# Kernel tuning notes

Measured on AMD Instinct MI355X. Metric: run time of the kernel, lower is better.

The kernel has to match this reference:

```python
import jax, jax.numpy as jnp
import numpy as np

N = 100000
E = 6400000
GAMMA = 1.0
SUPPORT = 0.05


def cohesion_kernel(q, h):
    # piecewise Akinci cohesion kernel (Cd normalization is unused in the original)
    qm1_3_q3 = (q - 1.0) ** 3 * q ** 3
    k1 = 128.0 * qm1_3_q3 + 1.0   # q <= 0.5
    k2 = 64.0 * qm1_3_q3           # q > 0.5
    return -jnp.where(q <= 0.5, k1, k2)


def kernel_gradient(q, dist, h):
    # 2D Wendland C2 kernel gradient: W = 7/(pi h^2) (1-q)^4 (1+4q)
    C = 7.0 / (np.pi * h ** 2)
    dWdq = C * (-20.0 * q * jnp.clip(1.0 - q, 0.0, None) ** 3) / h
    return dWdq[:, None] * dist  # [E,2]


def setup_inputs() -> dict:
    key = jax.random.key(0)
    k1, k2, k3, k4, k5, k6, k7 = jax.random.split(key, 7)
    neighbors = jnp.stack([
        jax.random.randint(k1, (E,), 0, N),
        jax.random.randint(k2, (E,), 0, N),
    ], axis=0)  # [2,E] int
    fluidAreas = jax.random.uniform(k3, (N,), dtype=jnp.float32)
    fluidDensities = jax.random.uniform(k4, (N,), dtype=jnp.float32) + 0.5  # avoid div-by-0
    fluidRestDensity = jax.random.uniform(k5, (N,), dtype=jnp.float32) + 0.5
    fluidRadialDistances = jax.random.uniform(k6, (E,), dtype=jnp.float32)  # q in [0,1]
    fluidDistances = jax.random.normal(k7, (E, 2), dtype=jnp.float32)
    # normalize to unit direction vectors as in the SPH pipeline
    fluidDistances = fluidDistances / (jnp.linalg.norm(fluidDistances, axis=1, keepdims=True) + 1e-7)
    return {
        'neighbors': neighbors,
        'fluidAreas': fluidAreas,
        'fluidDensities': fluidDensities,
        'fluidRestDensity': fluidRestDensity,
        'fluidRadialDistances': fluidRadialDistances,
        'fluidDistances': fluidDistances,
    }


def reference(neighbors, fluidAreas, fluidDensities, fluidRestDensity,
              fluidRadialDistances, fluidDistances):
    i = neighbors[0]
    j = neighbors[1]

    # computeNormalFunction
    fac_n = fluidAreas[j] / fluidDensities[j]                  # [E]
    grad = kernel_gradient(fluidRadialDistances, fluidDistances, SUPPORT)  # [E,2]
    normals = SUPPORT * jax.ops.segment_sum(fac_n[:, None] * grad, i, num_segments=N)  # [N,2]

    # computeCurvatureForce
    curvature = -GAMMA * jax.ops.segment_sum(normals[i] - normals[j], i, num_segments=N)

    # computeCohesionForce
    fac_c = fluidAreas[j] * fluidRestDensity[j]                # [E]
    kern = cohesion_kernel(fluidRadialDistances, SUPPORT)      # [E]
    cohesion = -GAMMA * jax.ops.segment_sum((fac_c * kern)[:, None] * fluidDistances, i, num_segments=N)

    # both forces are accumulated into fluidAcceleration
    return curvature + cohesion
```

## Files before the change

### kernel.cpp

```cpp
#include <hip/hip_runtime.h>

constexpr int N_PART = 100000;
constexpr int N_EDGE = 6400000;
constexpr float SUPPORT = 0.05f;
constexpr float PI_F = 3.14159265358979323846f;

constexpr int CH_LOG2 = 12;
constexpr int CH      = 1 << CH_LOG2;
constexpr int NCH     = (N_EDGE + CH - 1) / CH;
constexpr int BIN_LOG2 = 12;
constexpr int BINSZ   = 1 << BIN_LOG2;
constexpr int NBIN    = (N_PART + BINSZ - 1) / BINSZ;
constexpr int BT_STRIDE = 32;
constexpr int G_ACC   = 40;
constexpr int ST_NW   = 8;
constexpr int MAXC    = 48;

__global__ __launch_bounds__(512) void prep_fac(
    const float* __restrict__ areas,
    const float* __restrict__ dens,
    const float* __restrict__ rest,
    float2* __restrict__ fac)
{
    int p = blockIdx.x * blockDim.x + threadIdx.x;
    if (p < N_PART)
        fac[p] = make_float2(areas[p] / dens[p], areas[p] * rest[p]);
}

__global__ __launch_bounds__(256) void zero2(float* __restrict__ a,
                                             float* __restrict__ b, int n) {
    int idx = blockIdx.x * blockDim.x + threadIdx.x;
    if (idx < n) { a[idx] = 0.0f; b[idx] = 0.0f; }
}

__global__ __launch_bounds__(512) void l1_sort(
    const int* __restrict__ nb,
    const float2* __restrict__ fac,
    const float* __restrict__ q,
    const float2* __restrict__ dist,
    unsigned* __restrict__ gpack,
    float2* __restrict__ gpay1,
    float2* __restrict__ gpay2,
    unsigned* __restrict__ btab)
{
    __shared__ unsigned rec_pack[CH];
    __shared__ float    rec_q[CH];
    __shared__ float    rec_dx[CH];
    __shared__ float    rec_dy[CH];
    __shared__ unsigned hist[ST_NW * NBIN];
    __shared__ unsigned curw[ST_NW * NBIN];
    __shared__ unsigned base[NBIN + 1];
    __shared__ unsigned bcnt[NBIN];

    const int t   = blockIdx.x;
    const int c0  = t * CH;
    const int len = min(CH, N_EDGE - c0);
    const int tid = threadIdx.x;
    const int wid = tid >> 6;

    for (int k = tid; k < ST_NW * NBIN; k += 512) hist[k] = 0u;

    unsigned iv[8], jv[8];
    float    qv[8], dxv[8], dyv[8];
    #pragma unroll
    for (int k = 0; k < 8; ++k) {
        int idx = tid + k * 512;
        if (idx < len) {
            iv[k] = (unsigned)nb[c0 + idx];
            jv[k] = (unsigned)nb[N_EDGE + c0 + idx];
            qv[k] = q[c0 + idx];
            float2 d = dist[c0 + idx];
            dxv[k] = d.x;
            dyv[k] = d.y;
        }
    }
    __syncthreads();

    #pragma unroll
    for (int k = 0; k < 8; ++k) {
        int idx = tid + k * 512;
        if (idx < len)
            atomicAdd(&hist[wid * NBIN + (iv[k] >> BIN_LOG2)], 1u);
    }
    __syncthreads();

    if (tid < NBIN) {
        unsigned run = 0;
        for (int w = 0; w < ST_NW; ++w) {
            curw[w * NBIN + tid] = run;
            run += hist[w * NBIN + tid];
        }
        bcnt[tid] = run;
    }
    __syncthreads();
    if (tid == 0) {
        unsigned run = 0;
        for (int b = 0; b < NBIN; ++b) { base[b] = run; run += bcnt[b]; }
        base[NBIN] = run;
    }
    __syncthreads();
    if (tid < ST_NW * NBIN) curw[tid] += base[tid % NBIN];
    if (tid < NBIN)  btab[t * BT_STRIDE + tid]  = base[tid];
    if (tid == NBIN) btab[t * BT_STRIDE + NBIN] = (unsigned)len;
    __syncthreads();

    #pragma unroll
    for (int k = 0; k < 8; ++k) {
        int idx = tid + k * 512;
        if (idx < len) {
            unsigned i   = iv[k];
            unsigned bin = i >> BIN_LOG2;
            unsigned r = atomicAdd(&curw[wid * NBIN + bin], 1u) & (CH - 1);
            rec_pack[r] = ((i & (BINSZ - 1)) << 17) | jv[k];
            rec_q[r]    = qv[k];
            rec_dx[r]   = dxv[k];
            rec_dy[r]   = dyv[k];
        }
    }
    __syncthreads();

    const float Cw = 7.0f / (PI_F * SUPPORT * SUPPORT);
    for (int p = tid; p < len; p += 512) {
        unsigned pack = rec_pack[p];
        float qq = rec_q[p];
        float dx = rec_dx[p], dy = rec_dy[p];
        unsigned j = pack & 0x1FFFFu;
        float2 f = fac[j];

        float omq  = fmaxf(1.0f - qq, 0.0f);
        float dWdq = Cw * (-20.0f * qq * omq * omq * omq) * (1.0f / SUPPORT);
        float s    = SUPPORT * f.x * dWdq;

        float qm1  = qq - 1.0f;
        float tt   = qm1 * qm1 * qm1 * qq * qq * qq;
        float kern = (qq <= 0.5f) ? fmaf(128.0f, tt, 1.0f) : 64.0f * tt;
        float fc   = f.y * kern;

        int o = c0 + p;
        gpack[o] = pack;
        gpay1[o] = make_float2(s * dx, s * dy);
        gpay2[o] = make_float2(fc * dx, fc * dy);
    }
}

__global__ __launch_bounds__(512) void passB(
    const unsigned* __restrict__ btab,
    const unsigned* __restrict__ gpack,
    const float2* __restrict__ gpay1,
    float* __restrict__ gnorm)
{
    __shared__ float accx[BINSZ];
    __shared__ float accy[BINSZ];
    __shared__ unsigned s_sb[MAXC], s_se[MAXC], s_ln[MAXC];
    const int b = blockIdx.x % NBIN;
    const int g = blockIdx.x / NBIN;
    const int wave = threadIdx.x >> 6;
    const int lane = threadIdx.x & 63;

    const int t0 = (int)((long long)g * NCH / G_ACC);
    const int t1 = (int)((long long)(g + 1) * NCH / G_ACC);
    const int nt = t1 - t0;

    for (int k = threadIdx.x; k < BINSZ; k += 512) { accx[k] = 0.0f; accy[k] = 0.0f; }
    for (int c = threadIdx.x; c < nt; c += 512) {
        s_sb[c] = btab[(t0 + c) * BT_STRIDE + b];
        s_se[c] = btab[(t0 + c) * BT_STRIDE + b + 1];
        s_ln[c] = btab[(t0 + c) * BT_STRIDE + NBIN];
    }
    __syncthreads();

    for (int c = wave; c < nt; c += 8) {
        const int c0  = (t0 + c) * CH;
        const unsigned ln = min(s_ln[c], (unsigned)CH);
        unsigned sb = min(s_sb[c], ln);
        unsigned se = min(s_se[c], ln);
        for (unsigned k = sb + lane; k < se; k += 64) {
            int o = c0 + (int)k;
            unsigned pk = gpack[o];
            float2 p = gpay1[o];
            unsigned loc = (pk >> 17) & (BINSZ - 1);
            atomicAdd(&accx[loc], p.x);
            atomicAdd(&accy[loc], p.y);
        }
    }
    __syncthreads();

    const int gbase = b * BINSZ;
    for (int k = threadIdx.x; k < BINSZ; k += 512) {
        int p = gbase + k;
        if (p < N_PART) {
            atomicAdd(&gnorm[2 * p],     accx[k]);
            atomicAdd(&gnorm[2 * p + 1], accy[k]);
        }
    }
}

__global__ __launch_bounds__(512) void passD(
    const unsigned* __restrict__ btab,
    const unsigned* __restrict__ gpack,
    const float2* __restrict__ gpay2,
    const float2* __restrict__ normals,
    float* __restrict__ gout)
{
    __shared__ float accx[BINSZ];
    __shared__ float accy[BINSZ];
    __shared__ unsigned s_sb[MAXC], s_se[MAXC], s_ln[MAXC];
    const int b = blockIdx.x % NBIN;
    const int g = blockIdx.x / NBIN;
    const int wave = threadIdx.x >> 6;
    const int lane = threadIdx.x & 63;

    const int t0 = (int)((long long)g * NCH / G_ACC);
    const int t1 = (int)((long long)(g + 1) * NCH / G_ACC);
    const int nt = t1 - t0;

    for (int k = threadIdx.x; k < BINSZ; k += 512) { accx[k] = 0.0f; accy[k] = 0.0f; }
    for (int c = threadIdx.x; c < nt; c += 512) {
        s_sb[c] = btab[(t0 + c) * BT_STRIDE + b];
        s_se[c] = btab[(t0 + c) * BT_STRIDE + b + 1];
        s_ln[c] = btab[(t0 + c) * BT_STRIDE + NBIN];
    }
    __syncthreads();

    const int gbase = b * BINSZ;
    for (int c = wave; c < nt; c += 8) {
        const int c0  = (t0 + c) * CH;
        const unsigned ln = min(s_ln[c], (unsigned)CH);
        unsigned sb = min(s_sb[c], ln);
        unsigned se = min(s_se[c], ln);
        for (unsigned k = sb + lane; k < se; k += 64) {
            int o = c0 + (int)k;
            unsigned pk = gpack[o];
            float2 coh = gpay2[o];
            unsigned loc = (pk >> 17) & (BINSZ - 1);
            unsigned j   = min(pk & 0x1FFFFu, (unsigned)(N_PART - 1));
            unsigned ii  = min((unsigned)(gbase + loc), (unsigned)(N_PART - 1));
            float2 nj = normals[j];
            float2 ni = normals[ii];
            atomicAdd(&accx[loc], nj.x - ni.x + coh.x);
            atomicAdd(&accy[loc], nj.y - ni.y + coh.y);
        }
    }
    __syncthreads();

    for (int k = threadIdx.x; k < BINSZ; k += 512) {
        int p = gbase + k;
        if (p < N_PART) {
            atomicAdd(&gout[2 * p],     accx[k]);
            atomicAdd(&gout[2 * p + 1], accy[k]);
        }
    }
}

constexpr int FB_BSZ_LOG2 = 13;
constexpr int FB_BSZ   = 1 << FB_BSZ_LOG2;
constexpr int FB_NBINS = (N_PART + FB_BSZ - 1) / FB_BSZ;
constexpr int FB_NP_PAD = FB_NBINS * FB_BSZ;
constexpr int FB_C_TARGET = 39;

__global__ __launch_bounds__(1024) void fb_pass1_binned(
    const int* __restrict__ nb, const float* __restrict__ areas,
    const float* __restrict__ dens, const float* __restrict__ q,
    const float2* __restrict__ dist, float* __restrict__ partials, int C)
{
    __shared__ float lds[2 * FB_BSZ];
    const int b = blockIdx.x % FB_NBINS;
    const int c = blockIdx.x / FB_NBINS;
    for (int k = threadIdx.x; k < 2 * FB_BSZ; k += blockDim.x) lds[k] = 0.0f;
    __syncthreads();
    const int start = (int)((long long)c       * (N_EDGE / 4) / C) * 4;
    const int end   = (int)((long long)(c + 1) * (N_EDGE / 4) / C) * 4;
    const int4* __restrict__ nb4 = (const int4*)nb;
    const float Cw = 7.0f / (PI_F * SUPPORT * SUPPORT);
    for (int e = start + (int)threadIdx.x * 4; e < end; e += (int)blockDim.x * 4) {
        int4 iq = nb4[e >> 2];
        #pragma unroll
        for (int k = 0; k < 4; ++k) {
            int iv = (k == 0) ? iq.x : (k == 1) ? iq.y : (k == 2) ? iq.z : iq.w;
            if ((iv >> FB_BSZ_LOG2) == b) {
                int ee = e + k;
                int j  = nb[N_EDGE + ee];
                float qq  = q[ee];
                float fac = areas[j] / dens[j];
                float omq  = fmaxf(1.0f - qq, 0.0f);
                float dWdq = Cw * (-20.0f * qq * omq * omq * omq) * (1.0f / SUPPORT);
                float s = SUPPORT * fac * dWdq;
                float2 d = dist[ee];
                int loc = (iv & (FB_BSZ - 1)) << 1;
                atomicAdd(&lds[loc],     s * d.x);
                atomicAdd(&lds[loc + 1], s * d.y);
            }
        }
    }
    __syncthreads();
    float2* __restrict__ dst = (float2*)partials + (size_t)c * FB_NP_PAD + (size_t)b * FB_BSZ;
    const float2* __restrict__ src = (const float2*)lds;
    for (int k = threadIdx.x; k < FB_BSZ; k += blockDim.x) dst[k] = src[k];
}

__global__ __launch_bounds__(1024) void fb_pass2_binned(
    const int* __restrict__ nb, const float* __restrict__ areas,
    const float* __restrict__ rest, const float* __restrict__ q,
    const float2* __restrict__ dist, const float2* __restrict__ normals,
    float* __restrict__ partials, int C)
{
    __shared__ float lds[2 * FB_BSZ];
    const int b = blockIdx.x % FB_NBINS;
    const int c = blockIdx.x / FB_NBINS;
    for (int k = threadIdx.x; k < 2 * FB_BSZ; k += blockDim.x) lds[k] = 0.0f;
    __syncthreads();
    const int start = (int)((long long)c       * (N_EDGE / 4) / C) * 4;
    const int end   = (int)((long long)(c + 1) * (N_EDGE / 4) / C) * 4;
    const int4* __restrict__ nb4 = (const int4*)nb;
    for (int e = start + (int)threadIdx.x * 4; e < end; e += (int)blockDim.x * 4) {
        int4 iq = nb4[e >> 2];
        #pragma unroll
        for (int k = 0; k < 4; ++k) {
            int iv = (k == 0) ? iq.x : (k == 1) ? iq.y : (k == 2) ? iq.z : iq.w;
            if ((iv >> FB_BSZ_LOG2) == b) {
                int ee = e + k;
                int j  = nb[N_EDGE + ee];
                float2 ni = normals[iv];
                float2 nj = normals[j];
                float qq  = q[ee];
                float fc  = areas[j] * rest[j];
                float qm1 = qq - 1.0f;
                float t   = qm1 * qm1 * qm1 * qq * qq * qq;
                float kern = (qq <= 0.5f) ? fmaf(128.0f, t, 1.0f) : 64.0f * t;
                float2 d = dist[ee];
                int loc = (iv & (FB_BSZ - 1)) << 1;
                atomicAdd(&lds[loc],     -(ni.x - nj.x) + fc * kern * d.x);
                atomicAdd(&lds[loc + 1], -(ni.y - nj.y) + fc * kern * d.y);
            }
        }
    }
    __syncthreads();
    float2* __restrict__ dst = (float2*)partials + (size_t)c * FB_NP_PAD + (size_t)b * FB_BSZ;
    const float2* __restrict__ src = (const float2*)lds;
    for (int k = threadIdx.x; k < FB_BSZ; k += blockDim.x) dst[k] = src[k];
}

__global__ __launch_bounds__(256) void fb_reduce_partials(
    const float* __restrict__ partials, float* __restrict__ dst, int C)
{
    int p = blockIdx.x * blockDim.x + threadIdx.x;
    if (p >= N_PART) return;
    const float2* __restrict__ p2 = (const float2*)partials;
    float ax = 0.0f, ay = 0.0f;
    for (int c = 0; c < C; ++c) {
        float2 v = p2[(size_t)c * FB_NP_PAD + p];
        ax += v.x; ay += v.y;
    }
    ((float2*)dst)[p] = make_float2(ax, ay);
}

__global__ __launch_bounds__(256) void fb_pass1_atomic(
    const int* __restrict__ nb, const float* __restrict__ areas,
    const float* __restrict__ dens, const float* __restrict__ q,
    const float2* __restrict__ dist, float* __restrict__ normals)
{
    int e = blockIdx.x * blockDim.x + threadIdx.x;
    if (e >= N_EDGE) return;
    int i = nb[e];
    int j = nb[N_EDGE + e];
    float qq  = q[e];
    float fac = areas[j] / dens[j];
    const float Cw = 7.0f / (PI_F * SUPPORT * SUPPORT);
    float omq  = fmaxf(1.0f - qq, 0.0f);
    float dWdq = Cw * (-20.0f * qq * omq * omq * omq) * (1.0f / SUPPORT);
    float s = SUPPORT * fac * dWdq;
    float2 d = dist[e];
    atomicAdd(&normals[2 * i],     s * d.x);
    atomicAdd(&normals[2 * i + 1], s * d.y);
}

__global__ __launch_bounds__(256) void fb_pass2_atomic(
    const int* __restrict__ nb, const float* __restrict__ areas,
    const float* __restrict__ rest, const float* __restrict__ q,
    const float2* __restrict__ dist, const float2* __restrict__ normals,
    float* __restrict__ out)
{
    int e = blockIdx.x * blockDim.x + threadIdx.x;
    if (e >= N_EDGE) return;
    int i = nb[e];
    int j = nb[N_EDGE + e];
    float2 ni = normals[i];
    float2 nj = normals[j];
    float qq  = q[e];
    float fc  = areas[j] * rest[j];
    float qm1 = qq - 1.0f;
    float t   = qm1 * qm1 * qm1 * qq * qq * qq;
    float kern = (qq <= 0.5f) ? fmaf(128.0f, t, 1.0f) : 64.0f * t;
    float2 d = dist[e];
    atomicAdd(&out[2 * i],     -(ni.x - nj.x) + fc * kern * d.x);
    atomicAdd(&out[2 * i + 1], -(ni.y - nj.y) + fc * kern * d.y);
}

extern "C" void kernel_launch(void* const* d_in, const int* in_sizes, int n_in,
                              void* d_out, int out_size, void* d_ws, size_t ws_size,
                              hipStream_t stream) {
    const int*   nb    = (const int*)d_in[0];
    const float* areas = (const float*)d_in[1];
    const float* dens  = (const float*)d_in[2];
    const float* rest  = (const float*)d_in[3];
    const float* q     = (const float*)d_in[4];
    const float* dist  = (const float*)d_in[5];
    float* out = (float*)d_out;

    size_t off = 0;
    auto take = [&](size_t bytes) { size_t o = off; off += (bytes + 255) & ~(size_t)255; return o; };
    size_t o_pack    = take((size_t)N_EDGE * sizeof(unsigned));
    size_t o_pay1    = take((size_t)N_EDGE * sizeof(float2));
    size_t o_pay2    = take((size_t)N_EDGE * sizeof(float2));
    size_t o_btab    = take((size_t)NCH * BT_STRIDE * sizeof(unsigned));
    size_t o_normals = take((size_t)N_PART * sizeof(float2));
    size_t o_fac     = take((size_t)N_PART * sizeof(float2));
    size_t base_need = off;

    char* ws = (char*)d_ws;

    if (ws_size >= base_need) {
        unsigned* gpack   = (unsigned*)(ws + o_pack);
        float2*   gpay1   = (float2*)(ws + o_pay1);
        float2*   gpay2   = (float2*)(ws + o_pay2);
        unsigned* btab    = (unsigned*)(ws + o_btab);
        float2*   normals = (float2*)(ws + o_normals);
        float2*   fac     = (float2*)(ws + o_fac);

        zero2<<<(2 * N_PART + 255) / 256, 256, 0, stream>>>(
            (float*)normals, out, 2 * N_PART);
        prep_fac<<<(N_PART + 511) / 512, 512, 0, stream>>>(areas, dens, rest, fac);
        l1_sort<<<NCH, 512, 0, stream>>>(
            nb, fac, q, (const float2*)dist,
            gpack, gpay1, gpay2, btab);
        passB<<<NBIN * G_ACC, 512, 0, stream>>>(btab, gpack, gpay1, (float*)normals);
        passD<<<NBIN * G_ACC, 512, 0, stream>>>(btab, gpack, gpay2, normals, out);
        return;
    }

    const size_t normals_pad = 1 << 20;
    float* normals  = (float*)d_ws;
    float* partials = (float*)((char*)d_ws + normals_pad);
    const size_t per_chunk = (size_t)FB_NP_PAD * 2 * sizeof(float);
    int C = 0;
    if (ws_size > normals_pad) {
        C = (int)((ws_size - normals_pad) / per_chunk);
        if (C > FB_C_TARGET) C = FB_C_TARGET;
    }

    if (C >= 4) {
        const int grid = FB_NBINS * C;
        fb_pass1_binned<<<grid, 1024, 0, stream>>>(
            nb, areas, dens, q, (const float2*)dist, partials, C);
        fb_reduce_partials<<<(N_PART + 255) / 256, 256, 0, stream>>>(partials, normals, C);
        fb_pass2_binned<<<grid, 1024, 0, stream>>>(
            nb, areas, rest, q, (const float2*)dist, (const float2*)normals, partials, C);
        fb_reduce_partials<<<(N_PART + 255) / 256, 256, 0, stream>>>(partials, out, C);
    } else {
        const int nv = 2 * N_PART;
        zero2<<<(nv + 255) / 256, 256, 0, stream>>>(normals, out, nv);
        const int blocks = (N_EDGE + 255) / 256;
        fb_pass1_atomic<<<blocks, 256, 0, stream>>>(
            nb, areas, dens, q, (const float2*)dist, normals);
        fb_pass2_atomic<<<blocks, 256, 0, stream>>>(
            nb, areas, rest, q, (const float2*)dist, (const float2*)normals, out);
    }
}
```

Measured before the change: 389.0 us.

## Factor out self-normal term in curvature pass and unroll accumulation loops

In the curvature/cohesion pass, the per-edge gather of normals[i] is removed. Each bin instead counts its edges in a third LDS array and subtracts count*normals[i] once per particle at flush time. Both accumulation passes are unrolled by two to raise memory-level parallelism, and they drop the per-chunk length clamp. They also skip global atomics for all-zero bins and use unsafeAtomicAdd, and the passD grid split changes from 40 to 30 groups. The trade-offs are an extra LDS atomic per edge, slightly different floating-point rounding, and dependence on btab bounds being valid without the clamp.

```diff
diff --git a/kernel.cpp b/kernel.cpp
--- a/kernel.cpp
+++ b/kernel.cpp
@@ -12,9 +12,18 @@
 constexpr int BINSZ   = 1 << BIN_LOG2;
 constexpr int NBIN    = (N_PART + BINSZ - 1) / BINSZ;
 constexpr int BT_STRIDE = 32;
-constexpr int G_ACC   = 40;
+constexpr int G_B     = 40;
+constexpr int G_D     = 30;
 constexpr int ST_NW   = 8;
-constexpr int MAXC    = 48;
+constexpr int MAXC    = 56;
+
+__device__ __forceinline__ void gAdd(float* p, float v) {
+#if defined(__HIP_PLATFORM_AMD__) || defined(__HIP_PLATFORM_HCC__)
+    unsafeAtomicAdd(p, v);
+#else
+    atomicAdd(p, v);
+#endif
+}
 
 __global__ __launch_bounds__(512) void prep_fac(
     const float* __restrict__ areas,
@@ -151,30 +160,39 @@
 {
     __shared__ float accx[BINSZ];
     __shared__ float accy[BINSZ];
-    __shared__ unsigned s_sb[MAXC], s_se[MAXC], s_ln[MAXC];
+    __shared__ unsigned s_sb[MAXC], s_se[MAXC];
     const int b = blockIdx.x % NBIN;
     const int g = blockIdx.x / NBIN;
     const int wave = threadIdx.x >> 6;
     const int lane = threadIdx.x & 63;
 
-    const int t0 = (int)((long long)g * NCH / G_ACC);
-    const int t1 = (int)((long long)(g + 1) * NCH / G_ACC);
+    const int t0 = (int)((long long)g * NCH / G_B);
+    const int t1 = (int)((long long)(g + 1) * NCH / G_B);
     const int nt = t1 - t0;
 
     for (int k = threadIdx.x; k < BINSZ; k += 512) { accx[k] = 0.0f; accy[k] = 0.0f; }
     for (int c = threadIdx.x; c < nt; c += 512) {
         s_sb[c] = btab[(t0 + c) * BT_STRIDE + b];
         s_se[c] = btab[(t0 + c) * BT_STRIDE + b + 1];
-        s_ln[c] = btab[(t0 + c) * BT_STRIDE + NBIN];
     }
     __syncthreads();
 
     for (int c = wave; c < nt; c += 8) {
         const int c0  = (t0 + c) * CH;
-        const unsigned ln = min(s_ln[c], (unsigned)CH);
-        unsigned sb = min(s_sb[c], ln);
-        unsigned se = min(s_se[c], ln);
-        for (unsigned k = sb + lane; k < se; k += 64) {
+        unsigned sb = s_sb[c], se = s_se[c];
+        unsigned k = sb + lane;
+        for (; k + 64 < se; k += 128) {
+            int o0 = c0 + (int)k, o1 = o0 + 64;
+            unsigned pk0 = gpack[o0], pk1 = gpack[o1];
+            float2 p0 = gpay1[o0], p1 = gpay1[o1];
+            unsigned l0 = (pk0 >> 17) & (BINSZ - 1);
+            unsigned l1 = (pk1 >> 17) & (BINSZ - 1);
+            atomicAdd(&accx[l0], p0.x);
+            atomicAdd(&accy[l0], p0.y);
+            atomicAdd(&accx[l1], p1.x);
+            atomicAdd(&accy[l1], p1.y);
+        }
+        if (k < se) {
             int o = c0 + (int)k;
             unsigned pk = gpack[o];
             float2 p = gpay1[o];
@@ -189,8 +207,11 @@
     for (int k = threadIdx.x; k < BINSZ; k += 512) {
         int p = gbase + k;
         if (p < N_PART) {
-            atomicAdd(&gnorm[2 * p],     accx[k]);
-            atomicAdd(&gnorm[2 * p + 1], accy[k]);
+            float x = accx[k], y = accy[k];
+            if (x != 0.0f || y != 0.0f) {
+                gAdd(&gnorm[2 * p],     x);
+                gAdd(&gnorm[2 * p + 1], y);
+            }
         }
     }
 }
@@ -204,50 +225,71 @@
 {
     __shared__ float accx[BINSZ];
     __shared__ float accy[BINSZ];
-    __shared__ unsigned s_sb[MAXC], s_se[MAXC], s_ln[MAXC];
+    __shared__ float accd[BINSZ];
+    __shared__ unsigned s_sb[MAXC], s_se[MAXC];
     const int b = blockIdx.x % NBIN;
     const int g = blockIdx.x / NBIN;
     const int wave = threadIdx.x >> 6;
     const int lane = threadIdx.x & 63;
 
-    const int t0 = (int)((long long)g * NCH / G_ACC);
-    const int t1 = (int)((long long)(g + 1) * NCH / G_ACC);
+    const int t0 = (int)((long long)g * NCH / G_D);
+    const int t1 = (int)((long long)(g + 1) * NCH / G_D);
     const int nt = t1 - t0;
 
-    for (int k = threadIdx.x; k < BINSZ; k += 512) { accx[k] = 0.0f; accy[k] = 0.0f; }
+    for (int k = threadIdx.x; k < BINSZ; k += 512) {
+        accx[k] = 0.0f; accy[k] = 0.0f; accd[k] = 0.0f;
+    }
     for (int c = threadIdx.x; c < nt; c += 512) {
         s_sb[c] = btab[(t0 + c) * BT_STRIDE + b];
         s_se[c] = btab[(t0 + c) * BT_STRIDE + b + 1];
-        s_ln[c] = btab[(t0 + c) * BT_STRIDE + NBIN];
-    }
-    __syncthreads();
-
-    const int gbase = b * BINSZ;
+    }
+    __syncthreads();
+
     for (int c = wave; c < nt; c += 8) {
         const int c0  = (t0 + c) * CH;
-        const unsigned ln = min(s_ln[c], (unsigned)CH);
-        unsigned sb = min(s_sb[c], ln);
-        unsigned se = min(s_se[c], ln);
-        for (unsigned k = sb + lane; k < se; k += 64) {
+        unsigned sb = s_sb[c], se = s_se[c];
+        unsigned k = sb + lane;
+        for (; k + 64 < se; k += 128) {
+            int o0 = c0 + (int)k, o1 = o0 + 64;
+            unsigned pk0 = gpack[o0], pk1 = gpack[o1];
+            float2 h0 = gpay2[o0], h1 = gpay2[o1];
+            unsigned j0 = min(pk0 & 0x1FFFFu, (unsigned)(N_PART - 1));
+            unsigned j1 = min(pk1 & 0x1FFFFu, (unsigned)(N_PART - 1));
+            float2 nj0 = normals[j0];
+            float2 nj1 = normals[j1];
+            unsigned l0 = (pk0 >> 17) & (BINSZ - 1);
+            unsigned l1 = (pk1 >> 17) & (BINSZ - 1);
+            atomicAdd(&accx[l0], nj0.x + h0.x);
+            atomicAdd(&accy[l0], nj0.y + h0.y);
+            atomicAdd(&accd[l0], 1.0f);
+            atomicAdd(&accx[l1], nj1.x + h1.x);
+            atomicAdd(&accy[l1], nj1.y + h1.y);
+            atomicAdd(&accd[l1], 1.0f);
+        }
+        if (k < se) {
             int o = c0 + (int)k;
             unsigned pk = gpack[o];
             float2 coh = gpay2[o];
+            unsigned j   = min(pk & 0x1FFFFu, (unsigned)(N_PART - 1));
+            float2 nj = normals[j];
             unsigned loc = (pk >> 17) & (BINSZ - 1);
-            unsigned j   = min(pk & 0x1FFFFu, (unsigned)(N_PART - 1));
-            unsigned ii  = min((unsigned)(gbase + loc), (unsigned)(N_PART - 1));
-            float2 nj = normals[j];
-            float2 ni = normals[ii];
-            atomicAdd(&accx[loc], nj.x - ni.x + coh.x);
-            atomicAdd(&accy[loc], nj.y - ni.y + coh.y);
-        }
-    }
-    __syncthreads();
-
+            atomicAdd(&accx[loc], nj.x + coh.x);
+            atomicAdd(&accy[loc], nj.y + coh.y);
+            atomicAdd(&accd[loc], 1.0f);
+        }
+    }
+    __syncthreads();
+
+    const int gbase = b * BINSZ;
     for (int k = threadIdx.x; k < BINSZ; k += 512) {
         int p = gbase + k;
         if (p < N_PART) {
-            atomicAdd(&gout[2 * p],     accx[k]);
-            atomicAdd(&gout[2 * p + 1], accy[k]);
+            float d = accd[k];
+            if (d != 0.0f) {
+                float2 ni = normals[p];
+                gAdd(&gout[2 * p],     accx[k] - d * ni.x);
+                gAdd(&gout[2 * p + 1], accy[k] - d * ni.y);
+            }
         }
     }
 }
@@ -433,8 +475,8 @@
         l1_sort<<<NCH, 512, 0, stream>>>(
             nb, fac, q, (const float2*)dist,
             gpack, gpay1, gpay2, btab);
-        passB<<<NBIN * G_ACC, 512, 0, stream>>>(btab, gpack, gpay1, (float*)normals);
-        passD<<<NBIN * G_ACC, 512, 0, stream>>>(btab, gpack, gpay2, normals, out);
+        passB<<<NBIN * G_B, 512, 0, stream>>>(btab, gpack, gpay1, (float*)normals);
+        passD<<<NBIN * G_D, 512, 0, stream>>>(btab, gpack, gpay2, normals, out);
         return;
     }
 
```

Measured after the change: 400.6 us. +3.0%, slower.
